# Kernel optimization log

Hardware: AMD Instinct MI355X
Metric: run time of the kernel (lower is better)

Reference implementation:

```python
import jax, jax.numpy as jnp
import numpy as np

DEPTH, E, H, S, V, B = 6, 1024, 16, 2048, 32000, 2
HD = E // H
EPS = 1e-5


def _layernorm(x, w, b):
    mu = jnp.mean(x, axis=-1, keepdims=True)
    var = jnp.mean(jnp.square(x - mu), axis=-1, keepdims=True)
    return (x - mu) * jax.lax.rsqrt(var + EPS) * w + b


def setup_inputs() -> dict:
    key = jax.random.key(0)
    ks = jax.random.split(key, 8)
    std = 0.02
    return {
        "idx": jax.random.randint(ks[0], (B, S), 0, V),
        "tok_emb": jax.random.normal(ks[1], (V, E), jnp.float32) * std,
        "pos_emb": jax.random.normal(ks[2], (S, E), jnp.float32) * std,
        "qkv_w": jax.random.normal(ks[3], (DEPTH, 3 * E, E), jnp.float32) * std,
        "qkv_b": jnp.zeros((DEPTH, 3 * E), jnp.float32),
        "ln1_w": jnp.ones((DEPTH, E), jnp.float32),
        "ln1_b": jnp.zeros((DEPTH, E), jnp.float32),
        "ln2_w": jnp.ones((DEPTH, E), jnp.float32),
        "ln2_b": jnp.zeros((DEPTH, E), jnp.float32),
        "ff1_w": jax.random.normal(ks[4], (DEPTH, 4 * E, E), jnp.float32) * std,
        "ff1_b": jnp.zeros((DEPTH, 4 * E), jnp.float32),
        "ff2_w": jax.random.normal(ks[5], (DEPTH, E, 4 * E), jnp.float32) * std,
        "ff2_b": jnp.zeros((DEPTH, E), jnp.float32),
        "fin_w": jnp.ones((E,), jnp.float32),
        "fin_b": jnp.zeros((E,), jnp.float32),
        "proj_w": jax.random.normal(ks[6], (V, E), jnp.float32) * std,
    }


def _block(x, qkv_w, qkv_b, ln1_w, ln1_b, ln2_w, ln2_b, ff1_w, ff1_b, ff2_w, ff2_b):
    bs, seq, _ = x.shape
    # --- causal MSA (dropout in eval mode -> identity) ---
    xn = _layernorm(x, ln1_w, ln1_b)
    qkv = xn @ qkv_w.T + qkv_b                      # [B,S,3E]
    qkv = qkv.reshape(bs, seq, 3, H, HD)
    q, k, v = (jnp.moveaxis(qkv[:, :, i], 1, 2) for i in range(3))  # [B,H,S,HD]
    scores = jnp.einsum("bhqd,bhkd->bhqk", q, k) / jnp.sqrt(jnp.float32(HD))
    causal = jnp.triu(jnp.ones((seq, seq), bool), k=1)
    scores = jnp.where(causal[None, None], -jnp.inf, scores)
    probs = jax.nn.softmax(scores, axis=-1)
    attn = jnp.einsum("bhqk,bhkd->bqhd", probs, v).reshape(bs, seq, E)
    x = x + attn
    # --- feedforward ---
    xn = _layernorm(x, ln2_w, ln2_b)
    h = jax.nn.gelu(xn @ ff1_w.T + ff1_b, approximate=False)
    x = x + (h @ ff2_w.T + ff2_b)
    return x


def reference(idx, tok_emb, pos_emb, qkv_w, qkv_b, ln1_w, ln1_b, ln2_w, ln2_b,
              ff1_w, ff1_b, ff2_w, ff2_b, fin_w, fin_b, proj_w):
    bs, seq = idx.shape
    x = tok_emb[idx] + pos_emb[jnp.arange(seq)][None]  # [B,S,E]
    for l in range(DEPTH):
        x = _block(x, qkv_w[l], qkv_b[l], ln1_w[l], ln1_b[l], ln2_w[l], ln2_b[l],
                   ff1_w[l], ff1_b[l], ff2_w[l], ff2_b[l])
    x = _layernorm(x, fin_w, fin_b)
    logits = x @ proj_w.T  # [B,S,V], final_proj has no bias
    return logits
```

## Files before the change

### kernel.cpp

```cpp
#include <hip/hip_runtime.h>
#include <hip/hip_bf16.h>

#define DEPTH 6
#define E 1024
#define H 16
#define S 2048
#define V 32000
#define BB 2
#define HD 64
#define NTOK (BB * S)

typedef __attribute__((ext_vector_type(8))) short bf16x8;
typedef __attribute__((ext_vector_type(4))) float f32x4;
typedef unsigned short us;

__device__ inline us f2bf(float f) {
    union { float f; unsigned u; } v; v.f = f;
    unsigned r = v.u + 0x7fff + ((v.u >> 16) & 1);
    return (us)(r >> 16);
}
__device__ inline float bf2f(us b) {
    union { unsigned u; float f; } v; v.u = ((unsigned)b) << 16;
    return v.f;
}

__device__ __forceinline__ void gld16(const us* g, us* l) {
    __builtin_amdgcn_global_load_lds(
        (const __attribute__((address_space(1))) unsigned int*)g,
        (__attribute__((address_space(3))) unsigned int*)l, 16, 0, 0);
}

__global__ __launch_bounds__(256) void cast_kernel(const float* __restrict__ in,
                                                   us* __restrict__ out, int n8) {
    int i = blockIdx.x * 256 + threadIdx.x;
    if (i >= n8) return;
    const float4* p = (const float4*)in + 2 * (size_t)i;
    float4 a = p[0], b = p[1];
    uint4 o;
    o.x = f2bf(a.x) | ((unsigned)f2bf(a.y) << 16);
    o.y = f2bf(a.z) | ((unsigned)f2bf(a.w) << 16);
    o.z = f2bf(b.x) | ((unsigned)f2bf(b.y) << 16);
    o.w = f2bf(b.z) | ((unsigned)f2bf(b.w) << 16);
    ((uint4*)out)[i] = o;
}

__global__ void embed_kernel(const int* __restrict__ idx, const float* __restrict__ tok,
                             const float* __restrict__ pos, float* __restrict__ x) {
    int t = blockIdx.x;
    int s = t & (S - 1);
    int tokid = idx[t];
    int c = threadIdx.x * 4;
    float4 a = *(const float4*)&tok[(size_t)tokid * E + c];
    float4 p = *(const float4*)&pos[(size_t)s * E + c];
    float4 o; o.x = a.x + p.x; o.y = a.y + p.y; o.z = a.z + p.z; o.w = a.w + p.w;
    *(float4*)&x[(size_t)t * E + c] = o;
}

__global__ __launch_bounds__(256) void ln_kernel(const float* __restrict__ x,
                                                 const float* __restrict__ w,
                                                 const float* __restrict__ b,
                                                 us* __restrict__ out) {
    int row = blockIdx.x;
    int tid = threadIdx.x;
    int c = tid * 4;
    float4 v = *(const float4*)&x[(size_t)row * E + c];
    float s  = v.x + v.y + v.z + v.w;
    float sq = v.x * v.x + v.y * v.y + v.z * v.z + v.w * v.w;
    __shared__ float red[8];
    for (int o = 32; o > 0; o >>= 1) { s += __shfl_xor(s, o); sq += __shfl_xor(sq, o); }
    int wave = tid >> 6, lane = tid & 63;
    if (lane == 0) { red[wave] = s; red[4 + wave] = sq; }
    __syncthreads();
    if (tid == 0) {
        red[0] = red[0] + red[1] + red[2] + red[3];
        red[4] = red[4] + red[5] + red[6] + red[7];
    }
    __syncthreads();
    float mean = red[0] * (1.0f / E);
    float var  = red[4] * (1.0f / E) - mean * mean;
    float rstd = rsqrtf(var + 1e-5f);
    float4 wv = *(const float4*)&w[c];
    float4 bv = *(const float4*)&b[c];
    unsigned a0 = f2bf((v.x - mean) * rstd * wv.x + bv.x);
    unsigned a1 = f2bf((v.y - mean) * rstd * wv.y + bv.y);
    unsigned a2 = f2bf((v.z - mean) * rstd * wv.z + bv.z);
    unsigned a3 = f2bf((v.w - mean) * rstd * wv.w + bv.w);
    uint2 o; o.x = a0 | (a1 << 16); o.y = a2 | (a3 << 16);
    *(uint2*)&out[(size_t)row * E + c] = o;
}

__global__ __launch_bounds__(256) void combine_ln(const us* __restrict__ p0,
                                                  const us* __restrict__ p1,
                                                  const float* __restrict__ bias,
                                                  float* __restrict__ x,
                                                  const float* __restrict__ w,
                                                  const float* __restrict__ b,
                                                  us* __restrict__ out) {
    int row = blockIdx.x;
    int tid = threadIdx.x;
    int c = tid * 4;
    size_t base = (size_t)row * E + c;
    float4 v = *(const float4*)&x[base];
    uint2 a = *(const uint2*)&p0[base];
    uint2 bb2 = *(const uint2*)&p1[base];
    float4 bi = *(const float4*)&bias[c];
    v.x += bf2f((us)(a.x & 0xffff)) + bf2f((us)(bb2.x & 0xffff)) + bi.x;
    v.y += bf2f((us)(a.x >> 16))    + bf2f((us)(bb2.x >> 16))    + bi.y;
    v.z += bf2f((us)(a.y & 0xffff)) + bf2f((us)(bb2.y & 0xffff)) + bi.z;
    v.w += bf2f((us)(a.y >> 16))    + bf2f((us)(bb2.y >> 16))    + bi.w;
    *(float4*)&x[base] = v;

    float s  = v.x + v.y + v.z + v.w;
    float sq = v.x * v.x + v.y * v.y + v.z * v.z + v.w * v.w;
    __shared__ float red[8];
    for (int o = 32; o > 0; o >>= 1) { s += __shfl_xor(s, o); sq += __shfl_xor(sq, o); }
    int wave = tid >> 6, lane = tid & 63;
    if (lane == 0) { red[wave] = s; red[4 + wave] = sq; }
    __syncthreads();
    if (tid == 0) {
        red[0] = red[0] + red[1] + red[2] + red[3];
        red[4] = red[4] + red[5] + red[6] + red[7];
    }
    __syncthreads();
    float mean = red[0] * (1.0f / E);
    float var  = red[4] * (1.0f / E) - mean * mean;
    float rstd = rsqrtf(var + 1e-5f);
    float4 wv = *(const float4*)&w[c];
    float4 bv = *(const float4*)&b[c];
    unsigned a0 = f2bf((v.x - mean) * rstd * wv.x + bv.x);
    unsigned a1 = f2bf((v.y - mean) * rstd * wv.y + bv.y);
    unsigned a2 = f2bf((v.z - mean) * rstd * wv.z + bv.z);
    unsigned a3 = f2bf((v.w - mean) * rstd * wv.w + bv.w);
    uint2 o; o.x = a0 | (a1 << 16); o.y = a2 | (a3 << 16);
    *(uint2*)&out[base] = o;
}

#define GPH(dd, fb, STAGE, ISVM, IS12)                                              \
  {                                                                                 \
    bf16x8 afr0[2], afr1[2];                                                        \
    if ((fb) == 0) {                                                                \
      _Pragma("unroll")                                                             \
      for (int n = 0; n < 4; n++)                                                   \
        _Pragma("unroll")                                                           \
        for (int ks = 0; ks < 2; ks++)                                              \
          bfr[n][ks] = *(const bf16x8*)&lds[32768 + (dd) * 16384 +                  \
              (brow + n * 16) * 64 + ((ks * 4 + g4) ^ xg) * 8];                     \
    }                                                                               \
    _Pragma("unroll")                                                               \
    for (int ks = 0; ks < 2; ks++) {                                                \
      afr0[ks] = *(const bf16x8*)&lds[(dd) * 16384 + ((fb) >> 1) * 4096 +           \
          arow0 * 64 + ((ks * 4 + g4) ^ xg) * 8];                                   \
      afr1[ks] = *(const bf16x8*)&lds[(dd) * 16384 + ((fb) >> 1) * 4096 +           \
          arow1 * 64 + ((ks * 4 + g4) ^ xg) * 8];                                   \
    }                                                                               \
    STAGE;                                                                          \
    __builtin_amdgcn_sched_barrier(0);                                              \
    if (IS12) asm volatile("s_waitcnt lgkmcnt(8)" ::: "memory");                    \
    __builtin_amdgcn_s_barrier();                                                   \
    asm volatile("s_waitcnt lgkmcnt(0)" ::: "memory");                              \
    __builtin_amdgcn_sched_barrier(0);                                              \
    __builtin_amdgcn_s_setprio(1);                                                  \
    _Pragma("unroll")                                                               \
    for (int n = 0; n < 4; n++)                                                     \
      _Pragma("unroll")                                                             \
      for (int ks = 0; ks < 2; ks++) {                                              \
        acc[(fb)][n]     = __builtin_amdgcn_mfma_f32_16x16x32_bf16(afr0[ks], bfr[n][ks], acc[(fb)][n], 0, 0, 0);     \
        acc[(fb) + 1][n] = __builtin_amdgcn_mfma_f32_16x16x32_bf16(afr1[ks], bfr[n][ks], acc[(fb) + 1][n], 0, 0, 0); \
      }                                                                             \
    __builtin_amdgcn_s_setprio(0);                                                  \
    __builtin_amdgcn_sched_barrier(0);                                              \
    if (ISVM) asm volatile("s_waitcnt vmcnt(6)" ::: "memory");                      \
    __builtin_amdgcn_s_barrier();                                                   \
  }

template <int OUT_BF16, int ACT_GELU, int HAS_BIAS>
__global__ __launch_bounds__(512, 2) void gemm256(const us* __restrict__ A, int lda,
                                                  const us* __restrict__ Bw, int ldb,
                                                  const float* __restrict__ bias,
                                                  void* __restrict__ outp,
                                                  int M, int N, int K, int ldo) {
    __shared__ us lds[65536];
    int tid = threadIdx.x;
    int nwg = gridDim.x;
    int wgid = blockIdx.x;
    int chunk = nwg >> 3;
    int sw = (wgid & 7) * chunk + (wgid >> 3);
    int MB = M >> 8;
    int bm = (sw % MB) * 256;
    int bn = (sw / MB) * 256;
    int w = tid >> 6, lane = tid & 63;
    int wr = w >> 2, wc = w & 3;
    int l15 = lane & 15, g4 = lane >> 4;
    int xg = l15 & 7;
    int arow0 = (wr ? 32 : 0) + l15;
    int arow1 = arow0 + 16;
    int brow = wc * 64 + l15;
    int NT = K >> 6;

    f32x4 acc[8][4] = {};
    bf16x8 bfr[4][2];

    auto stA = [&](int u, int dd, int h) {
        int uu = (u < NT) ? u : NT - 1;
        #pragma unroll
        for (int i = 0; i < 2; i++) {
            int k = tid + i * 512;
            int q = 2 * h + (k >> 9);
            int r = (k >> 3) & 63;
            int tr = q * 32 + (r & 31) + ((r >> 5) << 7);
            int gp = (k & 7) ^ (r & 7);
            gld16(A + (size_t)(bm + tr) * lda + uu * 64 + gp * 8,
                  &lds[dd * 16384 + h * 8192 + k * 8]);
        }
    };
    auto stB = [&](int u, int dd, int h) {
        int uu = (u < NT) ? u : NT - 1;
        #pragma unroll
        for (int i = 0; i < 2; i++) {
            int k = tid + i * 512;
            int row = h * 128 + (k >> 3);
            int gp = (k & 7) ^ ((k >> 3) & 7);
            gld16(Bw + (size_t)(bn + row) * ldb + uu * 64 + gp * 8,
                  &lds[32768 + dd * 16384 + h * 8192 + k * 8]);
        }
    };

    stB(0, 0, 0); stB(0, 0, 1); stA(0, 0, 0); stA(0, 0, 1);
    stB(1, 1, 0); stB(1, 1, 1); stA(1, 1, 0);
    __builtin_amdgcn_sched_barrier(0);
    asm volatile("s_waitcnt vmcnt(6)" ::: "memory");
    __builtin_amdgcn_s_barrier();

    #pragma unroll 1
    for (int t = 0; t < NT; t += 2) {
        GPH(0, 0, stA(t + 1, 1, 1), 0, 1)
        GPH(0, 2, stB(t + 2, 0, 0), 0, 0)
        GPH(0, 4, stB(t + 2, 0, 1), 0, 0)
        GPH(0, 6, stA(t + 2, 0, 0), 1, 0)
        GPH(1, 0, stA(t + 2, 0, 1), 0, 1)
        GPH(1, 2, stB(t + 3, 1, 0), 0, 0)
        GPH(1, 4, stB(t + 3, 1, 1), 0, 0)
        GPH(1, 6, stA(t + 3, 1, 0), 1, 0)
    }

    float* outf = (float*)outp;
    us* outb = (us*)outp;
    #pragma unroll
    for (int mf = 0; mf < 8; mf++)
        #pragma unroll
        for (int n = 0; n < 4; n++)
            #pragma unroll
            for (int j = 0; j < 4; j++) {
                int r = bm + wr * 128 + mf * 16 + g4 * 4 + j;
                int c = bn + wc * 64 + n * 16 + l15;
                float v = acc[mf][n][j];
                if (HAS_BIAS) v += bias[c];
                if (ACT_GELU) v = 0.5f * v * (1.0f + erff(v * 0.70710678118f));
                if (OUT_BF16) outb[(size_t)r * ldo + c] = f2bf(v);
                else outf[(size_t)r * ldo + c] = v;
            }
}

template <int OUT_BF16, int ACT_GELU, int HAS_BIAS, int HAS_RES, int SPLITK>
__global__ __launch_bounds__(256) void gemm_bf16(const us* __restrict__ A, int lda,
                                                 const us* __restrict__ Bw, int ldb,
                                                 const float* __restrict__ bias,
                                                 const float* __restrict__ res,
                                                 void* __restrict__ outp,
                                                 int M, int N, int K, int ldo) {
    __shared__ us As[2 * 128 * 32];
    __shared__ us Bs[2 * 128 * 32];
    int tid = threadIdx.x;
    int nwg = gridDim.x;
    int chunk = nwg >> 3;
    int wgid = blockIdx.x;
    int sw = (wgid & 7) * chunk + (wgid >> 3);

    int bm, bn;
    us* outb = (us*)outp;
    float* outf = (float*)outp;
    if (SPLITK) {
        int kz = sw >> 8;
        int rem = sw & 255;
        bm = (rem & 31) * 128;
        bn = (rem >> 5) * 128;
        A  += (size_t)kz * K;
        Bw += (size_t)kz * K;
        outb += (size_t)kz * M * ldo;
    } else {
        int MB = M >> 7;
        bm = (sw % MB) * 128;
        bn = (sw / MB) * 128;
    }

    int wave = tid >> 6, lane = tid & 63;
    int wr = wave >> 1, wc = wave & 1;
    int l15 = lane & 15, g4 = lane >> 4;
    f32x4 acc[4][4] = {};

    for (int k0 = 0; k0 < K; k0 += 64) {
        #pragma unroll
        for (int p4 = 0; p4 < 4; p4++) {
            int p = p4 * 256 + tid;
            int ks = p >> 9, q = p & 511;
            int row = q >> 2, c8 = (q & 3) * 8;
            gld16(&A[(size_t)(bm + row) * lda + k0 + ks * 32 + c8], &As[p * 8]);
            gld16(&Bw[(size_t)(bn + row) * ldb + k0 + ks * 32 + c8], &Bs[p * 8]);
        }
        __syncthreads();
        bf16x8 a[4][2], bfr[4][2];
        #pragma unroll
        for (int m = 0; m < 4; m++)
            #pragma unroll
            for (int ks = 0; ks < 2; ks++)
                a[m][ks] = *(const bf16x8*)&As[ks * 4096 + (wr * 64 + m * 16 + l15) * 32 + g4 * 8];
        #pragma unroll
        for (int n = 0; n < 4; n++)
            #pragma unroll
            for (int ks = 0; ks < 2; ks++)
                bfr[n][ks] = *(const bf16x8*)&Bs[ks * 4096 + (wc * 64 + n * 16 + l15) * 32 + g4 * 8];
        #pragma unroll
        for (int m = 0; m < 4; m++)
            #pragma unroll
            for (int n = 0; n < 4; n++)
                #pragma unroll
                for (int ks = 0; ks < 2; ks++)
                    acc[m][n] = __builtin_amdgcn_mfma_f32_16x16x32_bf16(a[m][ks], bfr[n][ks], acc[m][n], 0, 0, 0);
        __syncthreads();
    }

    #pragma unroll
    for (int m = 0; m < 4; m++)
        #pragma unroll
        for (int n = 0; n < 4; n++)
            #pragma unroll
            for (int j = 0; j < 4; j++) {
                int r = bm + wr * 64 + m * 16 + g4 * 4 + j;
                int c = bn + wc * 64 + n * 16 + l15;
                float v = acc[m][n][j];
                if (HAS_BIAS) v += bias[c];
                if (ACT_GELU) v = 0.5f * v * (1.0f + erff(v * 0.70710678118f));
                if (HAS_RES) v += res[(size_t)r * ldo + c];
                if (OUT_BF16) outb[(size_t)r * ldo + c] = f2bf(v);
                else outf[(size_t)r * ldo + c] = v;
            }
}

__global__ __launch_bounds__(256) void transpose_v(const us* __restrict__ qkv,
                                                   us* __restrict__ vT) {
    int kt = blockIdx.x, h = blockIdx.y, b = blockIdx.z;
    int tid = threadIdx.x;
    __shared__ us T[64][72];
    const size_t base = (size_t)b * S * 3072 + 2048 + h * 64;
    int k0 = kt * 64;
    #pragma unroll
    for (int it = 0; it < 2; it++) {
        int p = tid + it * 256;
        int key = p & 63, c8 = (p >> 6) * 8;
        uint4 v = *(const uint4*)&qkv[base + (size_t)(k0 + key) * 3072 + c8];
        us* pv = (us*)&v;
        #pragma unroll
        for (int e = 0; e < 8; e++) T[c8 + e][key] = pv[e];
    }
    __syncthreads();
    const size_t obase = ((size_t)(b * H + h) * 64) * S + k0;
    #pragma unroll
    for (int it = 0; it < 2; it++) {
        int o = tid + it * 256;
        int d = o >> 3, cc = (o & 7) * 8;
        uint4 v = *(const uint4*)&T[d][cc];
        *(uint4*)&vT[obase + (size_t)d * S + cc] = v;
    }
}

__global__ __launch_bounds__(512, 4) void attn_kernel(const us* __restrict__ qkv,
                                                      const us* __restrict__ vT,
                                                      float* __restrict__ x) {
    int qt = blockIdx.x, h = blockIdx.y, b = blockIdx.z;
    int tid = threadIdx.x;
    int w = tid >> 6, lane = tid & 63;
    int l15 = lane & 15, g4 = lane >> 4;
    int s0 = qt * 128;
    int qrow_base = s0 + w * 16;
    const size_t qbase = (size_t)b * S * 3072;
    const size_t vtbase = ((size_t)(b * H + h) * 64) * S;

    __shared__ us K_lds[2][64 * 64];
    __shared__ us VT_lds[2][64 * 64];
    __shared__ us P_lds[8][16 * 72];

    bf16x8 q[2];
    #pragma unroll
    for (int dc = 0; dc < 2; dc++) {
        q[dc] = *(const bf16x8*)&qkv[qbase + (size_t)(qrow_base + l15) * 3072 + h * 64 + dc * 32 + 8 * g4];
        us* qq = (us*)&q[dc];
        #pragma unroll
        for (int e = 0; e < 8; e++) qq[e] = f2bf(bf2f(qq[e]) * 0.125f);
    }

    f32x4 O[4] = {};
    float m_run[4], l_run[4];
    #pragma unroll
    for (int j = 0; j < 4; j++) { m_run[j] = -INFINITY; l_run[j] = 0.0f; }

    int lastt = 2 * qt + 1;
    {
        int p = tid, row = p >> 3, cc = p & 7;
        int scc = cc ^ (row & 7);
        gld16(&qkv[qbase + (size_t)(0 + row) * 3072 + 1024 + h * 64 + scc * 8], &K_lds[0][p * 8]);
        gld16(&vT[vtbase + (size_t)row * S + 0 + scc * 8], &VT_lds[0][p * 8]);
    }
    __syncthreads();

    for (int t = 0; t <= lastt; t++) {
        int bb = t & 1;
        if (t < lastt) {
            int p = tid, row = p >> 3, cc = p & 7;
            int scc = cc ^ (row & 7);
            gld16(&qkv[qbase + (size_t)((t + 1) * 64 + row) * 3072 + 1024 + h * 64 + scc * 8], &K_lds[bb ^ 1][p * 8]);
            gld16(&vT[vtbase + (size_t)row * S + (t + 1) * 64 + scc * 8], &VT_lds[bb ^ 1][p * 8]);
        }
        int k0 = t * 64;
        if (k0 <= qrow_base + 15) {
            f32x4 sf[4];
            __builtin_amdgcn_s_setprio(1);
            #pragma unroll
            for (int c = 0; c < 4; c++) {
                f32x4 z = {};
                int row = c * 16 + l15;
                #pragma unroll
                for (int dc = 0; dc < 2; dc++) {
                    int ch = (dc * 4 + g4) ^ (row & 7);
                    bf16x8 kb = *(const bf16x8*)&K_lds[bb][row * 64 + ch * 8];
                    z = __builtin_amdgcn_mfma_f32_16x16x32_bf16(q[dc], kb, z, 0, 0, 0);
                }
                sf[c] = z;
            }
            __builtin_amdgcn_s_setprio(0);
            bool needmask = (k0 + 63 > qrow_base);
            float pr[4][4], alpha[4];
            #pragma unroll
            for (int j = 0; j < 4; j++) {
                int qrow = qrow_base + g4 * 4 + j;
                float v0 = sf[0][j], v1 = sf[1][j];
                float v2 = sf[2][j], v3 = sf[3][j];
                if (needmask) {
                    if (k0 +      l15 > qrow) v0 = -INFINITY;
                    if (k0 + 16 + l15 > qrow) v1 = -INFINITY;
                    if (k0 + 32 + l15 > qrow) v2 = -INFINITY;
                    if (k0 + 48 + l15 > qrow) v3 = -INFINITY;
                }
                float tm = fmaxf(fmaxf(v0, v1), fmaxf(v2, v3));
                tm = fmaxf(tm, __shfl_xor(tm, 1, 16));
                tm = fmaxf(tm, __shfl_xor(tm, 2, 16));
                tm = fmaxf(tm, __shfl_xor(tm, 4, 16));
                tm = fmaxf(tm, __shfl_xor(tm, 8, 16));
                float mnew = fmaxf(m_run[j], tm);
                float p0 = __expf(v0 - mnew), p1 = __expf(v1 - mnew);
                float p2 = __expf(v2 - mnew), p3 = __expf(v3 - mnew);
                float ts = (p0 + p1) + (p2 + p3);
                ts += __shfl_xor(ts, 1, 16);
                ts += __shfl_xor(ts, 2, 16);
                ts += __shfl_xor(ts, 4, 16);
                ts += __shfl_xor(ts, 8, 16);
                alpha[j] = __expf(m_run[j] - mnew);
                l_run[j] = l_run[j] * alpha[j] + ts;
                m_run[j] = mnew;
                pr[0][j] = p0; pr[1][j] = p1; pr[2][j] = p2; pr[3][j] = p3;
            }
            #pragma unroll
            for (int f = 0; f < 4; f++)
                #pragma unroll
                for (int j = 0; j < 4; j++) O[f][j] *= alpha[j];
            us* Pw = &P_lds[w][0];
            #pragma unroll
            for (int c = 0; c < 4; c++)
                #pragma unroll
                for (int j = 0; j < 4; j++)
                    Pw[(g4 * 4 + j) * 72 + c * 16 + l15] = f2bf(pr[c][j]);
            __builtin_amdgcn_s_setprio(1);
            #pragma unroll
            for (int kc = 0; kc < 2; kc++) {
                bf16x8 pa = *(const bf16x8*)&Pw[l15 * 72 + kc * 32 + g4 * 8];
                #pragma unroll
                for (int dt = 0; dt < 4; dt++) {
                    int row = dt * 16 + l15;
                    int ch = (kc * 4 + g4) ^ (row & 7);
                    bf16x8 vb = *(const bf16x8*)&VT_lds[bb][row * 64 + ch * 8];
                    O[dt] = __builtin_amdgcn_mfma_f32_16x16x32_bf16(pa, vb, O[dt], 0, 0, 0);
                }
            }
            __builtin_amdgcn_s_setprio(0);
        }
        __syncthreads();
    }
    #pragma unroll
    for (int dt = 0; dt < 4; dt++)
        #pragma unroll
        for (int j = 0; j < 4; j++) {
            size_t o = ((size_t)b * S + qrow_base + g4 * 4 + j) * E + h * 64 + dt * 16 + l15;
            x[o] += O[dt][j] / l_run[j];
        }
}

extern "C" void kernel_launch(void* const* d_in, const int* in_sizes, int n_in,
                              void* d_out, int out_size, void* d_ws, size_t ws_size,
                              hipStream_t stream) {
    const int*   idx    = (const int*)d_in[0];
    const float* tok    = (const float*)d_in[1];
    const float* pos    = (const float*)d_in[2];
    const float* qkv_w  = (const float*)d_in[3];
    const float* qkv_b  = (const float*)d_in[4];
    const float* ln1_w  = (const float*)d_in[5];
    const float* ln1_b  = (const float*)d_in[6];
    const float* ln2_w  = (const float*)d_in[7];
    const float* ln2_b  = (const float*)d_in[8];
    const float* ff1_w  = (const float*)d_in[9];
    const float* ff1_b  = (const float*)d_in[10];
    const float* ff2_w  = (const float*)d_in[11];
    const float* ff2_b  = (const float*)d_in[12];
    const float* fin_w  = (const float*)d_in[13];
    const float* fin_b  = (const float*)d_in[14];
    const float* proj_w = (const float*)d_in[15];

    char* ws = (char*)d_ws;
    float* x    = (float*)ws;
    us*    xn   = (us*)(ws + 16777216);
    us*    qkvb = (us*)(ws + 25165824);
    us*    hbuf = (us*)(ws + 50331648);
    us*    wbuf = (us*)(ws + 83886080);
    us*    vTb  = (us*)(ws + 92274688);
    us*    pbuf = qkvb;

    embed_kernel<<<NTOK, 256, 0, stream>>>(idx, tok, pos, x);
    ln_kernel<<<NTOK, 256, 0, stream>>>(x, ln1_w, ln1_b, xn);
    for (int l = 0; l < DEPTH; l++) {
        cast_kernel<<<1536, 256, 0, stream>>>(qkv_w + (size_t)l * 3 * E * E, wbuf, 3 * E * E / 8);
        gemm_bf16<1, 0, 1, 0, 0><<<768, 256, 0, stream>>>(
            xn, E, wbuf, E, qkv_b + l * 3 * E, nullptr, qkvb, NTOK, 3 * E, E, 3 * E);
        transpose_v<<<dim3(S / 64, H, BB), 256, 0, stream>>>(qkvb, vTb);
        attn_kernel<<<dim3(S / 128, H, BB), 512, 0, stream>>>(qkvb, vTb, x);
        ln_kernel<<<NTOK, 256, 0, stream>>>(x, ln2_w + l * E, ln2_b + l * E, xn);
        cast_kernel<<<2048, 256, 0, stream>>>(ff1_w + (size_t)l * 4 * E * E, wbuf, 4 * E * E / 8);
        gemm256<1, 1, 1><<<256, 512, 0, stream>>>(
            xn, E, wbuf, E, ff1_b + l * 4 * E, hbuf, NTOK, 4 * E, E, 4 * E);
        cast_kernel<<<2048, 256, 0, stream>>>(ff2_w + (size_t)l * E * 4 * E, wbuf, 4 * E * E / 8);
        gemm_bf16<1, 0, 0, 0, 1><<<512, 256, 0, stream>>>(
            hbuf, 4 * E, wbuf, 4 * E, nullptr, nullptr, qkvb, NTOK, E, 2 * E, E);
        const float* nw = (l < DEPTH - 1) ? (ln1_w + (l + 1) * E) : fin_w;
        const float* nb = (l < DEPTH - 1) ? (ln1_b + (l + 1) * E) : fin_b;
        combine_ln<<<NTOK, 256, 0, stream>>>(qkvb, qkvb + (size_t)NTOK * E, ff2_b + l * E,
                                             x, nw, nb, xn);
    }
    cast_kernel<<<16000, 256, 0, stream>>>(proj_w, pbuf, V * E / 8);
    gemm256<0, 0, 0><<<2000, 512, 0, stream>>>(
        xn, E, pbuf, E, nullptr, d_out, NTOK, V, E, V);
}
```

Before: 1.973 ms.

## Use 256-tile GEMM for QKV, split vocab projection, nontemporal logits stores

The QKV projection now uses the larger 256x256-tile gemm256 kernel with 192 workgroups instead of the 128-tile gemm_bf16 kernel with 768, trading more data reuse per tile for fewer workgroups. The vocab projection is split into two launches over column ranges of 16384 and 15616. This probably changes the workgroup-to-tile swizzle and keeps the B panel in cache better. Float output stores in gemm256 become nontemporal so the large logits tensor does not pollute the caches. gemm_bf16 is trimmed down to its split-K path only.

```diff
diff --git a/kernel.cpp b/kernel.cpp
--- a/kernel.cpp
+++ b/kernel.cpp
@@ -257,15 +257,13 @@
                 if (HAS_BIAS) v += bias[c];
                 if (ACT_GELU) v = 0.5f * v * (1.0f + erff(v * 0.70710678118f));
                 if (OUT_BF16) outb[(size_t)r * ldo + c] = f2bf(v);
-                else outf[(size_t)r * ldo + c] = v;
+                else __builtin_nontemporal_store(v, &outf[(size_t)r * ldo + c]);
             }
 }
 
-template <int OUT_BF16, int ACT_GELU, int HAS_BIAS, int HAS_RES, int SPLITK>
+template <int SPLITK>
 __global__ __launch_bounds__(256) void gemm_bf16(const us* __restrict__ A, int lda,
                                                  const us* __restrict__ Bw, int ldb,
-                                                 const float* __restrict__ bias,
-                                                 const float* __restrict__ res,
                                                  void* __restrict__ outp,
                                                  int M, int N, int K, int ldo) {
     __shared__ us As[2 * 128 * 32];
@@ -278,8 +276,7 @@
 
     int bm, bn;
     us* outb = (us*)outp;
-    float* outf = (float*)outp;
-    if (SPLITK) {
+    {
         int kz = sw >> 8;
         int rem = sw & 255;
         bm = (rem & 31) * 128;
@@ -287,10 +284,6 @@
         A  += (size_t)kz * K;
         Bw += (size_t)kz * K;
         outb += (size_t)kz * M * ldo;
-    } else {
-        int MB = M >> 7;
-        bm = (sw % MB) * 128;
-        bn = (sw / MB) * 128;
     }
 
     int wave = tid >> 6, lane = tid & 63;
@@ -337,12 +330,7 @@
             for (int j = 0; j < 4; j++) {
                 int r = bm + wr * 64 + m * 16 + g4 * 4 + j;
                 int c = bn + wc * 64 + n * 16 + l15;
-                float v = acc[m][n][j];
-                if (HAS_BIAS) v += bias[c];
-                if (ACT_GELU) v = 0.5f * v * (1.0f + erff(v * 0.70710678118f));
-                if (HAS_RES) v += res[(size_t)r * ldo + c];
-                if (OUT_BF16) outb[(size_t)r * ldo + c] = f2bf(v);
-                else outf[(size_t)r * ldo + c] = v;
+                outb[(size_t)r * ldo + c] = f2bf(acc[m][n][j]);
             }
 }
 
@@ -536,8 +524,8 @@
     ln_kernel<<<NTOK, 256, 0, stream>>>(x, ln1_w, ln1_b, xn);
     for (int l = 0; l < DEPTH; l++) {
         cast_kernel<<<1536, 256, 0, stream>>>(qkv_w + (size_t)l * 3 * E * E, wbuf, 3 * E * E / 8);
-        gemm_bf16<1, 0, 1, 0, 0><<<768, 256, 0, stream>>>(
-            xn, E, wbuf, E, qkv_b + l * 3 * E, nullptr, qkvb, NTOK, 3 * E, E, 3 * E);
+        gemm256<1, 0, 1><<<192, 512, 0, stream>>>(
+            xn, E, wbuf, E, qkv_b + l * 3 * E, qkvb, NTOK, 3 * E, E, 3 * E);
         transpose_v<<<dim3(S / 64, H, BB), 256, 0, stream>>>(qkvb, vTb);
         attn_kernel<<<dim3(S / 128, H, BB), 512, 0, stream>>>(qkvb, vTb, x);
         ln_kernel<<<NTOK, 256, 0, stream>>>(x, ln2_w + l * E, ln2_b + l * E, xn);
@@ -545,14 +533,16 @@
         gemm256<1, 1, 1><<<256, 512, 0, stream>>>(
             xn, E, wbuf, E, ff1_b + l * 4 * E, hbuf, NTOK, 4 * E, E, 4 * E);
         cast_kernel<<<2048, 256, 0, stream>>>(ff2_w + (size_t)l * E * 4 * E, wbuf, 4 * E * E / 8);
-        gemm_bf16<1, 0, 0, 0, 1><<<512, 256, 0, stream>>>(
-            hbuf, 4 * E, wbuf, 4 * E, nullptr, nullptr, qkvb, NTOK, E, 2 * E, E);
+        gemm_bf16<1><<<512, 256, 0, stream>>>(
+            hbuf, 4 * E, wbuf, 4 * E, qkvb, NTOK, E, 2 * E, E);
         const float* nw = (l < DEPTH - 1) ? (ln1_w + (l + 1) * E) : fin_w;
         const float* nb = (l < DEPTH - 1) ? (ln1_b + (l + 1) * E) : fin_b;
         combine_ln<<<NTOK, 256, 0, stream>>>(qkvb, qkvb + (size_t)NTOK * E, ff2_b + l * E,
                                              x, nw, nb, xn);
     }
     cast_kernel<<<16000, 256, 0, stream>>>(proj_w, pbuf, V * E / 8);
-    gemm256<0, 0, 0><<<2000, 512, 0, stream>>>(
-        xn, E, pbuf, E, nullptr, d_out, NTOK, V, E, V);
-}
+    gemm256<0, 0, 0><<<1024, 512, 0, stream>>>(
+        xn, E, pbuf, E, nullptr, d_out, NTOK, 16384, E, V);
+    gemm256<0, 0, 0><<<976, 512, 0, stream>>>(
+        xn, E, pbuf + (size_t)16384 * E, E, nullptr, (float*)d_out + 16384, NTOK, 15616, E, V);
+}
```

Measured after the change: 1.941 ms. No clear change (-1.7%).
